# Kernel optimization log

Measured on AMD Instinct MI355X. Metric: run time of the kernel, lower is better.

Reference implementation:

```python
import jax, jax.numpy as jnp
import numpy as np

B, S, D, P = 4, 2048, 1024, 1024

def setup_inputs() -> dict:
    key = jax.random.key(0)
    k1, k2, k3, k4 = jax.random.split(key, 4)
    x = jax.random.normal(k1, (B, S, D), dtype=jnp.float32)
    # nn.Linear weight is (out, in); store transposed (in, out) for x @ W
    scale = 1.0 / np.sqrt(D)
    Wq = jax.random.normal(k2, (D, P), dtype=jnp.float32) * scale
    Wk = jax.random.normal(k3, (D, P), dtype=jnp.float32) * scale
    Wv = jax.random.normal(k4, (D, P), dtype=jnp.float32) * scale
    return {"x": x, "Wq": Wq, "Wk": Wk, "Wv": Wv}

def reference(x, Wq, Wk, Wv):
    # projections (no bias)
    q = x @ Wq  # (B,S,P)
    k = x @ Wk
    v = x @ Wv
    scores = jnp.einsum('bsd,btd->bst', q, k)  # (B,S,S)
    seq = x.shape[1]
    causal = jnp.triu(jnp.ones((seq, seq), dtype=bool), k=1)
    scores = jnp.where(causal, -jnp.inf, scores)
    scores = scores / jnp.sqrt(jnp.asarray(P, dtype=scores.dtype))
    attn = jax.nn.softmax(scores, axis=-1)
    # dropout_prob=0.0 -> identity
    context = jnp.einsum('bst,btd->bsd', attn, v)  # (B,S,P)
    return context
```

## Files before the change

kernel.cpp:

```cpp
#include <hip/hip_runtime.h>
#include <hip/hip_bf16.h>


#define BDIM 4
#define SDIM 2048
#define DDIM 1024
#define PDIM 1024

typedef __attribute__((ext_vector_type(8))) short bf16x8;
typedef __attribute__((ext_vector_type(4))) float f32x4;
typedef __attribute__((ext_vector_type(16))) float f32x16;

__device__ __forceinline__ unsigned short f2bf(float f) {
    union { float f; unsigned int u; } v; v.f = f;
    unsigned int u = v.u;
    unsigned int r = (u + 0x7fffu + ((u >> 16) & 1u)) >> 16;
    return (unsigned short)r;
}

__device__ __forceinline__ float bf2f(unsigned short h) {
    union { unsigned int u; float f; } v;
    v.u = ((unsigned int)h) << 16;
    return v.f;
}

__device__ __forceinline__ void async16(const unsigned short* g, unsigned short* l) {
    __builtin_amdgcn_global_load_lds(
        (const __attribute__((address_space(1))) unsigned int*)g,
        (__attribute__((address_space(3))) unsigned int*)l,
        16, 0, 0);
}

__global__ __launch_bounds__(256) void prep_kernel(const float* __restrict__ x,
                                                   const float* __restrict__ W0,
                                                   const float* __restrict__ W1,
                                                   const float* __restrict__ W2,
                                                   unsigned short* __restrict__ Xb,
                                                   unsigned short* __restrict__ WT,
                                                   float* __restrict__ Lrow) {
    int bid = blockIdx.x;
    if (bid < 4096) {
        size_t i = (size_t)bid * 256 + threadIdx.x;
        float4 a = ((const float4*)x)[2 * i];
        float4 b = ((const float4*)x)[2 * i + 1];
        bf16x8 o;
        o[0] = (short)f2bf(a.x); o[1] = (short)f2bf(a.y);
        o[2] = (short)f2bf(a.z); o[3] = (short)f2bf(a.w);
        o[4] = (short)f2bf(b.x); o[5] = (short)f2bf(b.y);
        o[6] = (short)f2bf(b.z); o[7] = (short)f2bf(b.w);
        ((bf16x8*)Xb)[i] = o;
    } else if (bid < 4864) {
        int idx = bid - 4096;
        int wz = idx >> 8;
        int t  = idx & 255;
        const float* W = (wz == 0) ? W0 : (wz == 1) ? W1 : W2;
        unsigned short* Tz = WT + (size_t)wz * DDIM * PDIM;
        __shared__ float tle[64 * 65];
        int r0 = (t >> 4) * 64, c0 = (t & 15) * 64;
#pragma unroll
        for (int kk = 0; kk < 4; kk++) {
            int it = (int)threadIdx.x + 256 * kk;
            int r = it >> 4, c4 = (it & 15) * 4;
            float4 v = *(const float4*)(W + (size_t)(r0 + r) * PDIM + c0 + c4);
            float* dst = tle + r * 65 + c4;
            dst[0] = v.x; dst[1] = v.y; dst[2] = v.z; dst[3] = v.w;
        }
        __syncthreads();
#pragma unroll
        for (int kk = 0; kk < 2; kk++) {
            int it = (int)threadIdx.x + 256 * kk;
            int c = it >> 3, ch = (it & 7) * 8;
            bf16x8 o;
#pragma unroll
            for (int j = 0; j < 8; j++)
                o[j] = (short)f2bf(tle[(ch + j) * 65 + c]);
            *(bf16x8*)(Tz + (size_t)(c0 + c) * DDIM + r0 + ch) = o;
        }
    } else {
        float4 z4 = make_float4(0.f, 0.f, 0.f, 0.f);
#pragma unroll
        for (int kk = 0; kk < 8; kk++)
            ((float4*)Lrow)[(size_t)kk * 256 + threadIdx.x] = z4;
    }
}

template <int LDA, int LDB, int LDC, int KMAX, int MODE, typename CT>
__global__ __launch_bounds__(256) void gemm_bt(
    const unsigned short* __restrict__ A0, const unsigned short* __restrict__ A1,
    long long sA,
    const unsigned short* __restrict__ B0, long long sB,
    CT* __restrict__ C0, CT* __restrict__ C1, long long sC,
    unsigned short* __restrict__ Kb, unsigned short* __restrict__ VT,
    float* __restrict__ Lrow, float alpha) {
    const int BM = 128, BN = 128, BK = 64;
    const int ABUF = BM * BK;
    __shared__ __attribute__((aligned(16))) unsigned short smem[2 * ABUF + BN * BK];
    unsigned short* BsBuf = smem + 2 * ABUF;

    int tm, tn;
    if (MODE == 1) {
        int i = blockIdx.x;
        int t = (int)((sqrtf(8.f * i + 1.f) - 1.f) * 0.5f);
        if ((t + 1) * (t + 2) / 2 <= i) t++;
        if (t * (t + 1) / 2 > i) t--;
        tm = t * BM;
        tn = (i - t * (t + 1) / 2) * BN;
    } else if (MODE == 2) {
        int yy = (blockIdx.z < 2) ? ((int)gridDim.y - 1 - (int)blockIdx.y)
                                  : (int)blockIdx.y;
        tm = yy * BM;
        tn = blockIdx.x * BN;
    } else {
        tm = blockIdx.y * BM;
        tn = blockIdx.x * BN;
    }
    int kend = (MODE == 2) ? min(KMAX, tm + BM) : KMAX;

    int z = blockIdx.z;
    const unsigned short* A = (z < 2 ? A0 : A1) + (long long)(z & 1) * sA;
    const unsigned short* Bt = B0 + (long long)z * sB;
    CT* C = (z < 2 ? C0 : C1) + (long long)(z & 1) * sC;

    int tid  = threadIdx.x;
    int lane = tid & 63;
    int wave = tid >> 6;
    int wr   = (wave >> 1) * 64;
    int wc   = (wave & 1) * 64;
    int l31  = lane & 31;
    int hi   = lane >> 5;
    int rsw  = lane & 7;

    f32x16 acc[2][2] = {};

    int srow = tid >> 3;
    int scol = ((tid & 7) ^ (srow & 7)) * 8;
    const unsigned short* Ag = A + (size_t)(tm + srow) * LDA + scol;
    const unsigned short* Bg = Bt + (size_t)(tn + srow) * LDB + scol;

    auto issueA = [&](int k0, int buf) {
        unsigned short* la = smem + buf * ABUF + tid * 8;
        async16(Ag + k0, la);
        async16(Ag + k0 + 32 * LDA, la + 2048);
        async16(Ag + k0 + 64 * LDA, la + 4096);
        async16(Ag + k0 + 96 * LDA, la + 6144);
    };
    auto issueB = [&](int k0) {
        unsigned short* lb = BsBuf + tid * 8;
        async16(Bg + k0, lb);
        async16(Bg + k0 + 32 * LDB, lb + 2048);
        async16(Bg + k0 + 64 * LDB, lb + 4096);
        async16(Bg + k0 + 96 * LDB, lb + 6144);
    };

    auto kbody = [&](int i, int ns) {
        __syncthreads();
        bf16x8 bf[2][4];
#pragma unroll
        for (int nj = 0; nj < 2; nj++)
#pragma unroll
            for (int ks = 0; ks < 4; ks++)
                bf[nj][ks] = *(const bf16x8*)(BsBuf + (wc + nj * 32 + l31) * BK
                                                    + ((ks * 2 + hi) ^ rsw) * 8);
        __syncthreads();
        if (i + 1 < ns) { issueA((i + 1) * BK, (i + 1) & 1); issueB((i + 1) * BK); }
        const unsigned short* As = smem + (i & 1) * ABUF;
#pragma unroll
        for (int mi = 0; mi < 2; mi++) {
            bf16x8 af[4];
#pragma unroll
            for (int ks = 0; ks < 4; ks++)
                af[ks] = *(const bf16x8*)(As + (wr + mi * 32 + l31) * BK
                                             + ((ks * 2 + hi) ^ rsw) * 8);
#pragma unroll
            for (int ks = 0; ks < 4; ks++)
#pragma unroll
                for (int nj = 0; nj < 2; nj++)
                    acc[mi][nj] = __builtin_amdgcn_mfma_f32_32x32x16_bf16(
                        af[ks], bf[nj][ks], acc[mi][nj], 0, 0, 0);
        }
    };

    issueA(0, 0);
    issueB(0);
    if constexpr (MODE != 2) {
        constexpr int NS = KMAX / BK;
#pragma unroll
        for (int i = 0; i < NS; i++) kbody(i, NS);
    } else {
        int ns = kend / BK;
        for (int i = 0; i < ns; i++) kbody(i, ns);
    }

    if constexpr (MODE == 0) {
        if (tn < 2048) {
            unsigned short* D = (tn < 1024 ? (unsigned short*)C0 : Kb);
            int cbase = tn & 1023;
#pragma unroll
            for (int mi = 0; mi < 2; mi++) {
#pragma unroll
                for (int nj = 0; nj < 2; nj++) {
                    int c = cbase + wc + nj * 32 + l31;
#pragma unroll
                    for (int g = 0; g < 4; g++) {
                        int r0 = tm + wr + mi * 32 + g * 8 + hi * 4;
#pragma unroll
                        for (int rr = 0; rr < 4; rr++)
                            D[(size_t)(r0 + rr) * 1024 + c] =
                                f2bf(acc[mi][nj][g * 4 + rr]);
                    }
                }
            }
        } else {
            int b = tm >> 11;
            int s0 = tm & 2047;
            unsigned short* VTb = VT + (size_t)b * (PDIM * SDIM)
                                     + (size_t)(tn - 2048) * SDIM + s0;
            const int TP = 140;
            unsigned short* T = smem;
            __syncthreads();
#pragma unroll
            for (int q = 0; q < 2; q++) {
                if ((wave & 1) == q) {
#pragma unroll
                    for (int nj = 0; nj < 2; nj++) {
                        int cl = nj * 32 + l31;
#pragma unroll
                        for (int mi = 0; mi < 2; mi++) {
#pragma unroll
                            for (int g = 0; g < 4; g++) {
                                int rl = wr + mi * 32 + g * 8 + hi * 4;
                                ushort4 w;
                                w.x = f2bf(acc[mi][nj][g * 4 + 0]);
                                w.y = f2bf(acc[mi][nj][g * 4 + 1]);
                                w.z = f2bf(acc[mi][nj][g * 4 + 2]);
                                w.w = f2bf(acc[mi][nj][g * 4 + 3]);
                                *(ushort4*)(T + cl * TP + rl) = w;
                            }
                        }
                    }
                }
                __syncthreads();
                {
                    int lr = tid >> 2;
                    int ck = (tid & 3) * 32;
                    const unsigned short* Tr = T + lr * TP + ck;
                    ushort4 t0 = *(const ushort4*)(Tr + 0);
                    ushort4 t1 = *(const ushort4*)(Tr + 4);
                    ushort4 t2 = *(const ushort4*)(Tr + 8);
                    ushort4 t3 = *(const ushort4*)(Tr + 12);
                    ushort4 t4 = *(const ushort4*)(Tr + 16);
                    ushort4 t5 = *(const ushort4*)(Tr + 20);
                    ushort4 t6 = *(const ushort4*)(Tr + 24);
                    ushort4 t7 = *(const ushort4*)(Tr + 28);
                    bf16x8 u0, u1, u2, u3;
                    u0[0] = t0.x; u0[1] = t0.y; u0[2] = t0.z; u0[3] = t0.w;
                    u0[4] = t1.x; u0[5] = t1.y; u0[6] = t1.z; u0[7] = t1.w;
                    u1[0] = t2.x; u1[1] = t2.y; u1[2] = t2.z; u1[3] = t2.w;
                    u1[4] = t3.x; u1[5] = t3.y; u1[6] = t3.z; u1[7] = t3.w;
                    u2[0] = t4.x; u2[1] = t4.y; u2[2] = t4.z; u2[3] = t4.w;
                    u2[4] = t5.x; u2[5] = t5.y; u2[6] = t5.z; u2[7] = t5.w;
                    u3[0] = t6.x; u3[1] = t6.y; u3[2] = t6.z; u3[3] = t6.w;
                    u3[4] = t7.x; u3[5] = t7.y; u3[6] = t7.z; u3[7] = t7.w;
                    unsigned short* dst = VTb + (size_t)(64 * q + lr) * SDIM + ck;
                    *(bf16x8*)(dst) = u0;
                    *(bf16x8*)(dst + 8) = u1;
                    *(bf16x8*)(dst + 16) = u2;
                    *(bf16x8*)(dst + 24) = u3;
                }
                __syncthreads();
            }
        }
    } else if constexpr (MODE == 1) {
        float* Lb = Lrow + (size_t)z * SDIM;
        unsigned short* D = (unsigned short*)C;
#pragma unroll
        for (int mi = 0; mi < 2; mi++) {
#pragma unroll
            for (int g = 0; g < 4; g++) {
#pragma unroll
                for (int rr = 0; rr < 4; rr++) {
                    int r = tm + wr + mi * 32 + g * 8 + hi * 4 + rr;
                    float psum = 0.f;
#pragma unroll
                    for (int nj = 0; nj < 2; nj++) {
                        int c = tn + wc + nj * 32 + l31;
                        float p = 0.f;
                        if (c <= r)
                            p = __expf(acc[mi][nj][g * 4 + rr] * alpha - 8.0f);
                        psum += p;
                        D[(size_t)r * LDC + c] = f2bf(p);
                    }
#pragma unroll
                    for (int o = 16; o; o >>= 1) psum += __shfl_xor(psum, o, 64);
                    if (l31 == 0) atomicAdd(Lb + r, psum);
                }
            }
        }
    } else {
        const float* Lb = Lrow + (size_t)z * SDIM;
#pragma unroll
        for (int mi = 0; mi < 2; mi++) {
#pragma unroll
            for (int g = 0; g < 4; g++) {
#pragma unroll
                for (int rr = 0; rr < 4; rr++) {
                    int r = tm + wr + mi * 32 + g * 8 + hi * 4 + rr;
                    float inv = 1.0f / Lb[r];
#pragma unroll
                    for (int nj = 0; nj < 2; nj++) {
                        int c = tn + wc + nj * 32 + l31;
                        C[(size_t)r * LDC + c] = (CT)(acc[mi][nj][g * 4 + rr] * inv);
                    }
                }
            }
        }
    }
}

extern "C" void kernel_launch(void* const* d_in, const int* in_sizes, int n_in,
                              void* d_out, int out_size, void* d_ws, size_t ws_size,
                              hipStream_t stream) {
    const float* x  = (const float*)d_in[0];
    const float* Wq = (const float*)d_in[1];
    const float* Wk = (const float*)d_in[2];
    const float* Wv = (const float*)d_in[3];
    float* out = (float*)d_out;

    const size_t MS = (size_t)BDIM * SDIM;
    const long long SS = (long long)SDIM * SDIM;
    char* ws = (char*)d_ws;
    size_t off = 0;
    unsigned short* Xb   = (unsigned short*)(ws + off);
    unsigned short* S01  = Xb;                          off += MS * DDIM * 2;
    unsigned short* WT   = (unsigned short*)(ws + off); off += 3ull * DDIM * PDIM * 2;
    unsigned short* Q    = (unsigned short*)(ws + off); off += MS * PDIM * 2;
    unsigned short* Kb   = (unsigned short*)(ws + off); off += MS * PDIM * 2;
    unsigned short* VT   = (unsigned short*)(ws + off); off += MS * PDIM * 2;
    unsigned short* S23  = (unsigned short*)(ws + off); off += 2ull * SS * 2;
    float*          Lrow = (float*)(ws + off);          off += MS * sizeof(float);

    prep_kernel<<<4096 + 768 + 1, 256, 0, stream>>>(x, Wq, Wk, Wv, Xb, WT, Lrow);

    gemm_bt<DDIM, DDIM, PDIM, DDIM, 0, unsigned short>
        <<<dim3(3 * PDIM / 128, MS / 128, 1), 256, 0, stream>>>(
        Xb, Xb, 0, WT, 0, Q, Q, 0, Kb, VT, nullptr, 1.0f);

    const long long sQ = (long long)SDIM * PDIM;
    const float alpha = 1.0f / 32.0f;

    gemm_bt<PDIM, PDIM, SDIM, PDIM, 1, unsigned short>
        <<<dim3(136, 1, BDIM), 256, 0, stream>>>(
        Q, Q + 2 * sQ, sQ, Kb, sQ, S01, S23, SS, nullptr, nullptr, Lrow, alpha);

    const long long sOut = (long long)SDIM * PDIM;
    gemm_bt<SDIM, SDIM, PDIM, SDIM, 2, float>
        <<<dim3(PDIM / 128, SDIM / 128, BDIM), 256, 0, stream>>>(
        S01, S23, SS, VT, sQ, out, out + 2 * sOut, sOut, nullptr, nullptr, Lrow, 1.0f);
}
```

Before: 223.9 us.

## Overlap V projection with causal QK^T exp kernel in one launch

When the workspace is large enough, the projection GEMM now computes only Q and K. The V projection tiles (with transposed output) move into the same launch as the causal QK^T/exp kernel as extra blocks, and S01 goes to a separate buffer so Xb stays alive for the V blocks. This fills the GPU better during the triangular score kernel and removes a tail from the projection kernel. The cost is a larger workspace and a heterogeneous block mix that may contend for bandwidth.

After: 244.5 us. 9.2% more time.

```diff
diff --git a/kernel.cpp b/kernel.cpp
--- a/kernel.cpp
+++ b/kernel.cpp
@@ -16,12 +16,6 @@
     unsigned int u = v.u;
     unsigned int r = (u + 0x7fffu + ((u >> 16) & 1u)) >> 16;
     return (unsigned short)r;
-}
-
-__device__ __forceinline__ float bf2f(unsigned short h) {
-    union { unsigned int u; float f; } v;
-    v.u = ((unsigned int)h) << 16;
-    return v.f;
 }
 
 __device__ __forceinline__ void async16(const unsigned short* g, unsigned short* l) {
@@ -90,21 +84,32 @@
     long long sA,
     const unsigned short* __restrict__ B0, long long sB,
     CT* __restrict__ C0, CT* __restrict__ C1, long long sC,
-    unsigned short* __restrict__ Kb, unsigned short* __restrict__ VT,
-    float* __restrict__ Lrow, float alpha) {
+    const unsigned short* __restrict__ Wt, unsigned short* __restrict__ VT,
+    float* __restrict__ Lrow, float alpha, int nv) {
     const int BM = 128, BN = 128, BK = 64;
     const int ABUF = BM * BK;
     __shared__ __attribute__((aligned(16))) unsigned short smem[2 * ABUF + BN * BK];
     unsigned short* BsBuf = smem + 2 * ABUF;
 
     int tm, tn;
-    if (MODE == 1) {
-        int i = blockIdx.x;
-        int t = (int)((sqrtf(8.f * i + 1.f) - 1.f) * 0.5f);
-        if ((t + 1) * (t + 2) / 2 <= i) t++;
-        if (t * (t + 1) / 2 > i) t--;
-        tm = t * BM;
-        tn = (i - t * (t + 1) / 2) * BN;
+    int z = blockIdx.z;
+    bool vrole = false;
+    if constexpr (MODE == 3) {
+        int bid = blockIdx.x;
+        if (bid < nv) {
+            vrole = true;
+            tm = (bid >> 3) * BM;
+            tn = 2048 + (bid & 7) * BN;
+        } else {
+            int s = bid - nv;
+            z = s / 136;
+            int i = s % 136;
+            int t = (int)((sqrtf(8.f * i + 1.f) - 1.f) * 0.5f);
+            if ((t + 1) * (t + 2) / 2 <= i) t++;
+            if (t * (t + 1) / 2 > i) t--;
+            tm = t * BM;
+            tn = (i - t * (t + 1) / 2) * BN;
+        }
     } else if (MODE == 2) {
         int yy = (blockIdx.z < 2) ? ((int)gridDim.y - 1 - (int)blockIdx.y)
                                   : (int)blockIdx.y;
@@ -116,10 +121,23 @@
     }
     int kend = (MODE == 2) ? min(KMAX, tm + BM) : KMAX;
 
-    int z = blockIdx.z;
-    const unsigned short* A = (z < 2 ? A0 : A1) + (long long)(z & 1) * sA;
-    const unsigned short* Bt = B0 + (long long)z * sB;
-    CT* C = (z < 2 ? C0 : C1) + (long long)(z & 1) * sC;
+    const unsigned short* A;
+    const unsigned short* Bt;
+    CT* C = nullptr;
+    if constexpr (MODE == 3) {
+        if (vrole) {
+            A  = A1;
+            Bt = Wt;
+        } else {
+            A  = A0 + (long long)z * sA;
+            Bt = B0 + (long long)z * sB;
+            C  = (z < 2 ? C0 : C1) + (long long)(z & 1) * sC;
+        }
+    } else {
+        A  = (z < 2 ? A0 : A1) + (long long)(z & 1) * sA;
+        Bt = B0 + (long long)z * sB;
+        C  = (z < 2 ? C0 : C1) + (long long)(z & 1) * sC;
+    }
 
     int tid  = threadIdx.x;
     int lane = tid & 63;
@@ -191,9 +209,70 @@
         for (int i = 0; i < ns; i++) kbody(i, ns);
     }
 
+    auto v_transpose_out = [&]() {
+        int b = tm >> 11;
+        int s0 = tm & 2047;
+        unsigned short* VTb = VT + (size_t)b * (PDIM * SDIM)
+                                 + (size_t)(tn - 2048) * SDIM + s0;
+        const int TP = 140;
+        unsigned short* T = smem;
+        __syncthreads();
+#pragma unroll
+        for (int q = 0; q < 2; q++) {
+            if ((wave & 1) == q) {
+#pragma unroll
+                for (int nj = 0; nj < 2; nj++) {
+                    int cl = nj * 32 + l31;
+#pragma unroll
+                    for (int mi = 0; mi < 2; mi++) {
+#pragma unroll
+                        for (int g = 0; g < 4; g++) {
+                            int rl = wr + mi * 32 + g * 8 + hi * 4;
+                            ushort4 w;
+                            w.x = f2bf(acc[mi][nj][g * 4 + 0]);
+                            w.y = f2bf(acc[mi][nj][g * 4 + 1]);
+                            w.z = f2bf(acc[mi][nj][g * 4 + 2]);
+                            w.w = f2bf(acc[mi][nj][g * 4 + 3]);
+                            *(ushort4*)(T + cl * TP + rl) = w;
+                        }
+                    }
+                }
+            }
+            __syncthreads();
+            {
+                int lr = tid >> 2;
+                int ck = (tid & 3) * 32;
+                const unsigned short* Tr = T + lr * TP + ck;
+                ushort4 t0 = *(const ushort4*)(Tr + 0);
+                ushort4 t1 = *(const ushort4*)(Tr + 4);
+                ushort4 t2 = *(const ushort4*)(Tr + 8);
+                ushort4 t3 = *(const ushort4*)(Tr + 12);
+                ushort4 t4 = *(const ushort4*)(Tr + 16);
+                ushort4 t5 = *(const ushort4*)(Tr + 20);
+                ushort4 t6 = *(const ushort4*)(Tr + 24);
+                ushort4 t7 = *(const ushort4*)(Tr + 28);
+                bf16x8 u0, u1, u2, u3;
+                u0[0] = t0.x; u0[1] = t0.y; u0[2] = t0.z; u0[3] = t0.w;
+                u0[4] = t1.x; u0[5] = t1.y; u0[6] = t1.z; u0[7] = t1.w;
+                u1[0] = t2.x; u1[1] = t2.y; u1[2] = t2.z; u1[3] = t2.w;
+                u1[4] = t3.x; u1[5] = t3.y; u1[6] = t3.z; u1[7] = t3.w;
+                u2[0] = t4.x; u2[1] = t4.y; u2[2] = t4.z; u2[3] = t4.w;
+                u2[4] = t5.x; u2[5] = t5.y; u2[6] = t5.z; u2[7] = t5.w;
+                u3[0] = t6.x; u3[1] = t6.y; u3[2] = t6.z; u3[3] = t6.w;
+                u3[4] = t7.x; u3[5] = t7.y; u3[6] = t7.z; u3[7] = t7.w;
+                unsigned short* dst = VTb + (size_t)(64 * q + lr) * SDIM + ck;
+                *(bf16x8*)(dst) = u0;
+                *(bf16x8*)(dst + 8) = u1;
+                *(bf16x8*)(dst + 16) = u2;
+                *(bf16x8*)(dst + 24) = u3;
+            }
+            __syncthreads();
+        }
+    };
+
     if constexpr (MODE == 0) {
         if (tn < 2048) {
-            unsigned short* D = (tn < 1024 ? (unsigned short*)C0 : Kb);
+            unsigned short* D = (tn < 1024 ? (unsigned short*)C0 : (unsigned short*)C1);
             int cbase = tn & 1023;
 #pragma unroll
             for (int mi = 0; mi < 2; mi++) {
@@ -211,88 +290,35 @@
                 }
             }
         } else {
-            int b = tm >> 11;
-            int s0 = tm & 2047;
-            unsigned short* VTb = VT + (size_t)b * (PDIM * SDIM)
-                                     + (size_t)(tn - 2048) * SDIM + s0;
-            const int TP = 140;
-            unsigned short* T = smem;
-            __syncthreads();
-#pragma unroll
-            for (int q = 0; q < 2; q++) {
-                if ((wave & 1) == q) {
-#pragma unroll
-                    for (int nj = 0; nj < 2; nj++) {
-                        int cl = nj * 32 + l31;
-#pragma unroll
-                        for (int mi = 0; mi < 2; mi++) {
-#pragma unroll
-                            for (int g = 0; g < 4; g++) {
-                                int rl = wr + mi * 32 + g * 8 + hi * 4;
-                                ushort4 w;
-                                w.x = f2bf(acc[mi][nj][g * 4 + 0]);
-                                w.y = f2bf(acc[mi][nj][g * 4 + 1]);
-                                w.z = f2bf(acc[mi][nj][g * 4 + 2]);
-                                w.w = f2bf(acc[mi][nj][g * 4 + 3]);
-                                *(ushort4*)(T + cl * TP + rl) = w;
-                            }
+            v_transpose_out();
+        }
+    } else if constexpr (MODE == 3) {
+        if (vrole) {
+            v_transpose_out();
+        } else {
+            float* Lb = Lrow + (size_t)z * SDIM;
+            unsigned short* D = (unsigned short*)C;
+#pragma unroll
+            for (int mi = 0; mi < 2; mi++) {
+#pragma unroll
+                for (int g = 0; g < 4; g++) {
+#pragma unroll
+                    for (int rr = 0; rr < 4; rr++) {
+                        int r = tm + wr + mi * 32 + g * 8 + hi * 4 + rr;
+                        float psum = 0.f;
+#pragma unroll
+                        for (int nj = 0; nj < 2; nj++) {
+                            int c = tn + wc + nj * 32 + l31;
+                            float p = 0.f;
+                            if (c <= r)
+                                p = __expf(acc[mi][nj][g * 4 + rr] * alpha - 8.0f);
+                            psum += p;
+                            D[(size_t)r * LDC + c] = f2bf(p);
                         }
+#pragma unroll
+                        for (int o = 16; o; o >>= 1) psum += __shfl_xor(psum, o, 64);
+                        if (l31 == 0) atomicAdd(Lb + r, psum);
                     }
-                }
-                __syncthreads();
-                {
-                    int lr = tid >> 2;
-                    int ck = (tid & 3) * 32;
-                    const unsigned short* Tr = T + lr * TP + ck;
-                    ushort4 t0 = *(const ushort4*)(Tr + 0);
-                    ushort4 t1 = *(const ushort4*)(Tr + 4);
-                    ushort4 t2 = *(const ushort4*)(Tr + 8);
-                    ushort4 t3 = *(const ushort4*)(Tr + 12);
-                    ushort4 t4 = *(const ushort4*)(Tr + 16);
-                    ushort4 t5 = *(const ushort4*)(Tr + 20);
-                    ushort4 t6 = *(const ushort4*)(Tr + 24);
-                    ushort4 t7 = *(const ushort4*)(Tr + 28);
-                    bf16x8 u0, u1, u2, u3;
-                    u0[0] = t0.x; u0[1] = t0.y; u0[2] = t0.z; u0[3] = t0.w;
-                    u0[4] = t1.x; u0[5] = t1.y; u0[6] = t1.z; u0[7] = t1.w;
-                    u1[0] = t2.x; u1[1] = t2.y; u1[2] = t2.z; u1[3] = t2.w;
-                    u1[4] = t3.x; u1[5] = t3.y; u1[6] = t3.z; u1[7] = t3.w;
-                    u2[0] = t4.x; u2[1] = t4.y; u2[2] = t4.z; u2[3] = t4.w;
-                    u2[4] = t5.x; u2[5] = t5.y; u2[6] = t5.z; u2[7] = t5.w;
-                    u3[0] = t6.x; u3[1] = t6.y; u3[2] = t6.z; u3[3] = t6.w;
-                    u3[4] = t7.x; u3[5] = t7.y; u3[6] = t7.z; u3[7] = t7.w;
-                    unsigned short* dst = VTb + (size_t)(64 * q + lr) * SDIM + ck;
-                    *(bf16x8*)(dst) = u0;
-                    *(bf16x8*)(dst + 8) = u1;
-                    *(bf16x8*)(dst + 16) = u2;
-                    *(bf16x8*)(dst + 24) = u3;
-                }
-                __syncthreads();
-            }
-        }
-    } else if constexpr (MODE == 1) {
-        float* Lb = Lrow + (size_t)z * SDIM;
-        unsigned short* D = (unsigned short*)C;
-#pragma unroll
-        for (int mi = 0; mi < 2; mi++) {
-#pragma unroll
-            for (int g = 0; g < 4; g++) {
-#pragma unroll
-                for (int rr = 0; rr < 4; rr++) {
-                    int r = tm + wr + mi * 32 + g * 8 + hi * 4 + rr;
-                    float psum = 0.f;
-#pragma unroll
-                    for (int nj = 0; nj < 2; nj++) {
-                        int c = tn + wc + nj * 32 + l31;
-                        float p = 0.f;
-                        if (c <= r)
-                            p = __expf(acc[mi][nj][g * 4 + rr] * alpha - 8.0f);
-                        psum += p;
-                        D[(size_t)r * LDC + c] = f2bf(p);
-                    }
-#pragma unroll
-                    for (int o = 16; o; o >>= 1) psum += __shfl_xor(psum, o, 64);
-                    if (l31 == 0) atomicAdd(Lb + r, psum);
                 }
             }
         }
@@ -329,31 +355,42 @@
     const size_t MS = (size_t)BDIM * SDIM;
     const long long SS = (long long)SDIM * SDIM;
     char* ws = (char*)d_ws;
+
     size_t off = 0;
-    unsigned short* Xb   = (unsigned short*)(ws + off);
-    unsigned short* S01  = Xb;                          off += MS * DDIM * 2;
+    unsigned short* Xb   = (unsigned short*)(ws + off); off += MS * DDIM * 2;
     unsigned short* WT   = (unsigned short*)(ws + off); off += 3ull * DDIM * PDIM * 2;
     unsigned short* Q    = (unsigned short*)(ws + off); off += MS * PDIM * 2;
     unsigned short* Kb   = (unsigned short*)(ws + off); off += MS * PDIM * 2;
     unsigned short* VT   = (unsigned short*)(ws + off); off += MS * PDIM * 2;
     unsigned short* S23  = (unsigned short*)(ws + off); off += 2ull * SS * 2;
     float*          Lrow = (float*)(ws + off);          off += MS * sizeof(float);
-
-    prep_kernel<<<4096 + 768 + 1, 256, 0, stream>>>(x, Wq, Wk, Wv, Xb, WT, Lrow);
-
-    gemm_bt<DDIM, DDIM, PDIM, DDIM, 0, unsigned short>
-        <<<dim3(3 * PDIM / 128, MS / 128, 1), 256, 0, stream>>>(
-        Xb, Xb, 0, WT, 0, Q, Q, 0, Kb, VT, nullptr, 1.0f);
+    size_t off_base = off;
+    bool big = (ws_size >= off_base + 2ull * SS * 2);
+    unsigned short* S01 = big ? (unsigned short*)(ws + off_base) : Xb;
 
     const long long sQ = (long long)SDIM * PDIM;
     const float alpha = 1.0f / 32.0f;
 
-    gemm_bt<PDIM, PDIM, SDIM, PDIM, 1, unsigned short>
-        <<<dim3(136, 1, BDIM), 256, 0, stream>>>(
-        Q, Q + 2 * sQ, sQ, Kb, sQ, S01, S23, SS, nullptr, nullptr, Lrow, alpha);
+    prep_kernel<<<4096 + 768 + 1, 256, 0, stream>>>(x, Wq, Wk, Wv, Xb, WT, Lrow);
+
+    if (big) {
+        gemm_bt<DDIM, DDIM, PDIM, DDIM, 0, unsigned short>
+            <<<dim3(2048 / 128, MS / 128, 1), 256, 0, stream>>>(
+            Xb, Xb, 0, WT, 0, Q, Kb, 0, nullptr, VT, nullptr, 1.0f, 0);
+        gemm_bt<PDIM, PDIM, SDIM, PDIM, 3, unsigned short>
+            <<<dim3(512 + 544, 1, 1), 256, 0, stream>>>(
+            Q, Xb, sQ, Kb, sQ, S01, S23, SS, WT, VT, Lrow, alpha, 512);
+    } else {
+        gemm_bt<DDIM, DDIM, PDIM, DDIM, 0, unsigned short>
+            <<<dim3(3 * PDIM / 128, MS / 128, 1), 256, 0, stream>>>(
+            Xb, Xb, 0, WT, 0, Q, Kb, 0, nullptr, VT, nullptr, 1.0f, 0);
+        gemm_bt<PDIM, PDIM, SDIM, PDIM, 3, unsigned short>
+            <<<dim3(544, 1, 1), 256, 0, stream>>>(
+            Q, Xb, sQ, Kb, sQ, S01, S23, SS, WT, VT, Lrow, alpha, 0);
+    }
 
     const long long sOut = (long long)SDIM * PDIM;
     gemm_bt<SDIM, SDIM, PDIM, SDIM, 2, float>
         <<<dim3(PDIM / 128, SDIM / 128, BDIM), 256, 0, stream>>>(
-        S01, S23, SS, VT, sQ, out, out + 2 * sOut, sOut, nullptr, nullptr, Lrow, 1.0f);
-}
+        S01, S23, SS, VT, sQ, out, out + 2 * sOut, sOut, nullptr, nullptr, Lrow, 1.0f, 0);
+}
```
